# Kernel tuning notes

Hardware: AMD Instinct MI355X
Metric: run time of the kernel (lower is better)

The kernel has to match this reference:

```python
import jax, jax.numpy as jnp
import numpy as np

HEADS = 8
RANK = 4

def _lora(x, w_down, w_up, palette, in_dim, out_dim):
    # w_down: [RANK*in_dim, 15], w_up: [RANK*out_dim, 15], palette: [1, 15]
    down = (palette @ w_down.T).reshape(RANK, in_dim)   # [r, in]
    up = (palette @ w_up.T).reshape(out_dim, RANK)      # [out, r]
    return (x @ down.T) @ up.T                          # [..., out]


def setup_inputs() -> dict:
    key = jax.random.key(0)
    ks = jax.random.split(key, 16)
    B, S, D = 2, 2048, 1280
    def n(k, shape, std=0.02):
        return (jax.random.normal(k, shape, dtype=jnp.float32) * std).astype(jnp.float32)
    return {
        'hidden_states': jax.random.normal(ks[0], (B, S, D), dtype=jnp.float32),
        'color_palette': jax.random.uniform(ks[1], (1, 15), dtype=jnp.float32),
        'Wq': n(ks[2], (D, D)), 'Wk': n(ks[3], (D, D)),
        'Wv': n(ks[4], (D, D)), 'Wo': n(ks[5], (D, D)),
        'bo': jnp.zeros((D,), dtype=jnp.float32),
        'q_down': n(ks[6], (RANK * D, 15), 0.25), 'q_up': n(ks[7], (RANK * D, 15)),
        'k_down': n(ks[8], (RANK * D, 15), 0.25), 'k_up': n(ks[9], (RANK * D, 15)),
        'v_down': n(ks[10], (RANK * D, 15), 0.25), 'v_up': n(ks[11], (RANK * D, 15)),
        'o_down': n(ks[12], (RANK * D, 15), 0.25), 'o_up': n(ks[13], (RANK * D, 15)),
    }


def reference(hidden_states, color_palette, Wq, Wk, Wv, Wo, bo,
              q_down, q_up, k_down, k_up, v_down, v_up, o_down, o_up):
    B, S, D = hidden_states.shape
    H = HEADS
    hd = D // H
    scale = 1.0  # LoRA scale
    x = hidden_states
    # LoRA-augmented projections (self-attention: encoder_hidden_states = x)
    q = x @ Wq.T + scale * _lora(x, q_down, q_up, color_palette, D, D)
    k = x @ Wk.T + scale * _lora(x, k_down, k_up, color_palette, D, D)
    v = x @ Wv.T + scale * _lora(x, v_down, v_up, color_palette, D, D)
    # split heads: [B, S, D] -> [B, H, S, hd]
    q = q.reshape(B, S, H, hd).transpose(0, 2, 1, 3)
    k = k.reshape(B, S, H, hd).transpose(0, 2, 1, 3)
    v = v.reshape(B, S, H, hd).transpose(0, 2, 1, 3)
    attn_scale = 1.0 / jnp.sqrt(jnp.asarray(hd, dtype=q.dtype))
    scores = jnp.einsum('bhqd,bhkd->bhqk', q, k) * attn_scale
    probs = jax.nn.softmax(scores, axis=-1)
    out = jnp.einsum('bhqk,bhkd->bhqd', probs, v)
    out = out.transpose(0, 2, 1, 3).reshape(B, S, D)
    out = out @ Wo.T + bo + scale * _lora(out, o_down, o_up, color_palette, D, D)
    return out
```

## Files before the change

kernel.cpp:

```cpp
#include <hip/hip_runtime.h>

typedef unsigned short u16;
typedef unsigned int u32;
typedef __attribute__((ext_vector_type(4))) float floatx4;
typedef __attribute__((ext_vector_type(8))) __bf16 bf16x8;

#define MFMA_BF16(a, b, c) __builtin_amdgcn_mfma_f32_16x16x32_bf16((a), (b), (c), 0, 0, 0)

typedef const __attribute__((address_space(1))) void* gas_ptr;
typedef __attribute__((address_space(3))) void* las_ptr;

__device__ __forceinline__ void gll16(const void* g, void* l) {
  __builtin_amdgcn_global_load_lds((gas_ptr)g, (las_ptr)l, 16, 0, 0);
}

__device__ __forceinline__ u16 f2bf(float x) {
  u32 u = __builtin_bit_cast(u32, x);
  u = (u + 0x7fffu + ((u >> 16) & 1u)) >> 16;
  return (u16)u;
}

__global__ void prep_downup(const float* __restrict__ pal,
                            const float* __restrict__ qd, const float* __restrict__ qu,
                            const float* __restrict__ kd, const float* __restrict__ ku,
                            const float* __restrict__ vd, const float* __restrict__ vu,
                            const float* __restrict__ od, const float* __restrict__ ou,
                            float* __restrict__ down_f, float* __restrict__ up_f) {
  int tid = blockIdx.x * blockDim.x + threadIdx.x;
  int w = tid / 10240;
  int rem = tid - w * 10240;
  const float* dsrc = (w == 0) ? qd : (w == 1) ? kd : (w == 2) ? vd : od;
  const float* usrc = (w == 0) ? qu : (w == 1) ? ku : (w == 2) ? vu : ou;
  bool isdown = rem < 5120;
  int row = isdown ? rem : rem - 5120;
  const float* src = (isdown ? dsrc : usrc) + row * 15;
  float s = 0.f;
#pragma unroll
  for (int p = 0; p < 15; ++p) s += pal[p] * src[p];
  if (isdown) down_f[w * 5120 + row] = s;
  else        up_f[w * 5120 + row] = s;
}

__global__ void build_weff(const float* __restrict__ Wq, const float* __restrict__ Wk,
                           const float* __restrict__ Wv, const float* __restrict__ Wo,
                           const float* __restrict__ down_f, const float* __restrict__ up_f,
                           u16* __restrict__ weff_qkv, u16* __restrict__ weff_o) {
  int tid = blockIdx.x * blockDim.x + threadIdx.x;
  int w = tid / 1638400;
  int rem = tid - w * 1638400;
  int n = rem / 1280;
  int k = rem - n * 1280;
  const float* W = (w == 0) ? Wq : (w == 1) ? Wk : (w == 2) ? Wv : Wo;
  const float* up = up_f + w * 5120 + n * 4;
  const float* dn = down_f + w * 5120 + k;
  float v = W[rem] + up[0] * dn[0] + up[1] * dn[1280] + up[2] * dn[2560] + up[3] * dn[3840];
  u16 hv = f2bf(v);
  if (w < 3) weff_qkv[w * 1638400 + rem] = hv;
  else       weff_o[rem] = hv;
}

__global__ void cvt_x(const float4* __restrict__ x, ushort4* __restrict__ xb) {
  int i = blockIdx.x * blockDim.x + threadIdx.x;
  float4 v = x[i];
  ushort4 o;
  o.x = f2bf(v.x); o.y = f2bf(v.y); o.z = f2bf(v.z); o.w = f2bf(v.w);
  xb[i] = o;
}

__global__ __launch_bounds__(256) void gemm128_qkv(const u16* __restrict__ A, const u16* __restrict__ Bm,
                                                   u16* __restrict__ qb, u16* __restrict__ kb,
                                                   u16* __restrict__ vbuf, int K) {
  __shared__ __align__(16) u16 lA[128 * 64];
  __shared__ __align__(16) u16 lB[128 * 64];
  const int t = threadIdx.x;
  const int lane = t & 63;
  const int l15 = lane & 15, quad = lane >> 4;
  const int wid = t >> 6;
  const int wm = (wid >> 1) * 64;
  const int wn = (wid & 1) * 64;
  const int bm = blockIdx.x * 128;
  const int bn = blockIdx.y * 128;
  floatx4 acc[4][4] = {};

  int soff[4];
#pragma unroll
  for (int i = 0; i < 4; ++i) {
    int c = t + i * 256;
    int row = c >> 3, pos = c & 7;
    soff[i] = row * K + ((pos + row) & 7) * 8;
  }
  int afo[4][2], bfo[4][2];
#pragma unroll
  for (int i = 0; i < 4; ++i) {
#pragma unroll
    for (int ch = 0; ch < 2; ++ch) {
      int ra = wm + i * 16 + l15;
      int rb = wn + i * 16 + l15;
      int kc8 = ch * 4 + quad;
      afo[i][ch] = ra * 64 + ((kc8 - ra) & 7) * 8;
      bfo[i][ch] = rb * 64 + ((kc8 - rb) & 7) * 8;
    }
  }

  const u16* Ab = A + (long)bm * K;
  const u16* Bb = Bm + (long)bn * K;
  const int nkt = K >> 6;

  for (int kt = 0; kt < nkt; ++kt) {
    __syncthreads();
    const int k0 = kt * 64;
#pragma unroll
    for (int i = 0; i < 4; ++i) gll16(Ab + (long)soff[i] + k0, lA + (t + i * 256) * 8);
#pragma unroll
    for (int i = 0; i < 4; ++i) gll16(Bb + (long)soff[i] + k0, lB + (t + i * 256) * 8);
    __syncthreads();
#pragma unroll
    for (int ch = 0; ch < 2; ++ch) {
      bf16x8 af[4], bfr[4];
#pragma unroll
      for (int i = 0; i < 4; ++i) af[i] = *(const bf16x8*)(lA + afo[i][ch]);
#pragma unroll
      for (int i = 0; i < 4; ++i) bfr[i] = *(const bf16x8*)(lB + bfo[i][ch]);
#pragma unroll
      for (int i = 0; i < 4; ++i)
#pragma unroll
        for (int j = 0; j < 4; ++j)
          acc[i][j] = MFMA_BF16(af[i], bfr[j], acc[i][j]);
    }
  }

#pragma unroll
  for (int i = 0; i < 4; ++i) {
#pragma unroll
    for (int j = 0; j < 4; ++j) {
#pragma unroll
      for (int r = 0; r < 4; ++r) {
        int m = bm + wm + i * 16 + quad * 4 + r;
        int n = bn + wn + j * 16 + l15;
        u16 hv = f2bf(acc[i][j][r]);
        if (n < 1280) {
          qb[(long)m * 1280 + n] = hv;
        } else if (n < 2560) {
          kb[(long)m * 1280 + (n - 1280)] = hv;
        } else {
          vbuf[(long)m * 1280 + (n - 2560)] = hv;
        }
      }
    }
  }
}

__global__ __launch_bounds__(256) void vtrans(const u16* __restrict__ vbuf,
                                              u16* __restrict__ vtb) {
  __shared__ u16 tile[64 * 65];
  const int t = threadIdx.x;
  const int sb = blockIdx.x * 64, nb = blockIdx.y * 64, b = blockIdx.z;
  const u16* src = vbuf + ((long)(b * 2048 + sb)) * 1280 + nb;
#pragma unroll
  for (int it = 0; it < 16; ++it) {
    int idx = t + it * 256;
    int s = idx >> 6, n = idx & 63;
    tile[s * 65 + n] = src[(long)s * 1280 + n];
  }
  __syncthreads();
  u16* dst = vtb + ((long)(b * 1280 + nb)) * 2048 + sb;
#pragma unroll
  for (int it = 0; it < 16; ++it) {
    int idx = t + it * 256;
    int n = idx >> 6, s = idx & 63;
    dst[(long)n * 2048 + s] = tile[s * 65 + n];
  }
}

__global__ __launch_bounds__(256) void gemm64_o(const u16* __restrict__ A, const u16* __restrict__ Bm,
                                                float* __restrict__ outf,
                                                const float* __restrict__ bias, int K) {
  __shared__ __align__(16) u16 lA[64 * 64];
  __shared__ __align__(16) u16 lB[128 * 64];
  const int t = threadIdx.x;
  const int lane = t & 63;
  const int l15 = lane & 15, quad = lane >> 4;
  const int wid = t >> 6;
  const int bm = blockIdx.x * 64;
  const int bn = blockIdx.y * 128;
  floatx4 acc[4][2] = {};

  int aoff[2], boff[4];
#pragma unroll
  for (int i = 0; i < 2; ++i) {
    int c = t + i * 256;
    int row = c >> 3, pos = c & 7;
    aoff[i] = row * K + ((pos + row) & 7) * 8;
  }
#pragma unroll
  for (int i = 0; i < 4; ++i) {
    int c = t + i * 256;
    int row = c >> 3, pos = c & 7;
    boff[i] = row * K + ((pos + row) & 7) * 8;
  }
  int afo[4][2], bfo[2][2];
#pragma unroll
  for (int ch = 0; ch < 2; ++ch) {
    int kc8 = ch * 4 + quad;
#pragma unroll
    for (int i = 0; i < 4; ++i) {
      int ra = i * 16 + l15;
      afo[i][ch] = ra * 64 + ((kc8 - ra) & 7) * 8;
    }
#pragma unroll
    for (int j = 0; j < 2; ++j) {
      int rb = wid * 32 + j * 16 + l15;
      bfo[j][ch] = rb * 64 + ((kc8 - rb) & 7) * 8;
    }
  }

  const u16* Ab = A + (long)bm * K;
  const u16* Bb = Bm + (long)bn * K;
  const int nkt = K >> 6;

  for (int kt = 0; kt < nkt; ++kt) {
    __syncthreads();
    const int k0 = kt * 64;
#pragma unroll
    for (int i = 0; i < 2; ++i) gll16(Ab + (long)aoff[i] + k0, lA + (t + i * 256) * 8);
#pragma unroll
    for (int i = 0; i < 4; ++i) gll16(Bb + (long)boff[i] + k0, lB + (t + i * 256) * 8);
    __syncthreads();
#pragma unroll
    for (int ch = 0; ch < 2; ++ch) {
      bf16x8 af[4], bfr[2];
#pragma unroll
      for (int i = 0; i < 4; ++i) af[i] = *(const bf16x8*)(lA + afo[i][ch]);
#pragma unroll
      for (int j = 0; j < 2; ++j) bfr[j] = *(const bf16x8*)(lB + bfo[j][ch]);
#pragma unroll
      for (int i = 0; i < 4; ++i)
#pragma unroll
        for (int j = 0; j < 2; ++j)
          acc[i][j] = MFMA_BF16(af[i], bfr[j], acc[i][j]);
    }
  }

#pragma unroll
  for (int i = 0; i < 4; ++i) {
#pragma unroll
    for (int j = 0; j < 2; ++j) {
#pragma unroll
      for (int r = 0; r < 4; ++r) {
        int m = bm + i * 16 + quad * 4 + r;
        int n = bn + wid * 32 + j * 16 + l15;
        outf[(long)m * 1280 + n] = acc[i][j][r] + bias[n];
      }
    }
  }
}

__global__ __launch_bounds__(256) void flash_attn(const u16* __restrict__ qb,
                                                  const u16* __restrict__ kb,
                                                  const u16* __restrict__ vtb,
                                                  u16* __restrict__ attn) {
  const int S = 2048, D = 1280, HD = 160;
  __shared__ __align__(16) u16 kt_lds[64 * 160];
  __shared__ __align__(16) u16 vt_lds[160 * 64];
  __shared__ __align__(16) u16 p_lds[4][16 * 76];
  const int t = threadIdx.x, lane = t & 63, wid = t >> 6;
  const int quad = lane >> 4, l15 = lane & 15;
  const int bh = blockIdx.y, b = bh >> 3, h = bh & 7;
  const int q0 = blockIdx.x * 64 + wid * 16;
  const float kS = 0.11404582025f;

  bf16x8 aq[5];
  {
    const u16* qg = qb + ((long)(b * 2048 + q0 + l15)) * D + h * HD + quad * 8;
#pragma unroll
    for (int dc = 0; dc < 5; ++dc) aq[dc] = *(const bf16x8*)(qg + dc * 32);
  }

  const u16* kg[5];
  const u16* vg[5];
  {
    const u16* kgbase = kb + ((long)(b * 2048)) * D + h * HD;
    const u16* vgbase = vtb + ((long)(b * 1280 + h * HD)) * 2048;
#pragma unroll
    for (int i = 0; i < 5; ++i) {
      int c = t + i * 256;
      int key = c / 20, rot = c - key * 20;
      int ccol = rot - (key % 20);
      if (ccol < 0) ccol += 20;
      kg[i] = kgbase + (long)key * D + ccol * 8;
      int vrow = c >> 3, swz = c & 7;
      int vcol = swz ^ (vrow & 7);
      vg[i] = vgbase + (long)vrow * 2048 + vcol * 8;
    }
  }

  int kfo[4][5];
#pragma unroll
  for (int j = 0; j < 4; ++j) {
    int key = j * 16 + l15;
    int r0 = (quad + key) % 20;
#pragma unroll
    for (int dc = 0; dc < 5; ++dc) {
      int rot = r0 + dc * 4;
      if (rot >= 20) rot -= 20;
      kfo[j][dc] = (key * 20 + rot) * 8;
    }
  }
  int vfo[10][2];
#pragma unroll
  for (int dc = 0; dc < 10; ++dc) {
    int row = dc * 16 + l15;
#pragma unroll
    for (int ks = 0; ks < 2; ++ks) {
      int sw = (ks * 4 + quad) ^ (row & 7);
      vfo[dc][ks] = (row * 8 + sw) * 8;
    }
  }

  float l_part[4] = {0.f, 0.f, 0.f, 0.f};
  floatx4 o_acc[10] = {};

  for (int kt0 = 0; kt0 < S; kt0 += 64) {
    __syncthreads();
#pragma unroll
    for (int i = 0; i < 5; ++i) gll16(kg[i], kt_lds + (t + i * 256) * 8);
#pragma unroll
    for (int i = 0; i < 5; ++i) gll16(vg[i], vt_lds + (t + i * 256) * 8);
#pragma unroll
    for (int i = 0; i < 5; ++i) { kg[i] += (long)64 * D; vg[i] += 64; }
    __syncthreads();

    floatx4 s[4] = {};
#pragma unroll
    for (int dc = 0; dc < 5; ++dc) {
#pragma unroll
      for (int j = 0; j < 4; ++j) {
        bf16x8 kf = *(const bf16x8*)(kt_lds + kfo[j][dc]);
        s[j] = MFMA_BF16(aq[dc], kf, s[j]);
      }
    }

#pragma unroll
    for (int r = 0; r < 4; ++r) {
      float p0 = __builtin_exp2f(fminf(s[0][r] * kS, 80.f));
      float p1 = __builtin_exp2f(fminf(s[1][r] * kS, 80.f));
      float p2 = __builtin_exp2f(fminf(s[2][r] * kS, 80.f));
      float p3 = __builtin_exp2f(fminf(s[3][r] * kS, 80.f));
      l_part[r] += (p0 + p1) + (p2 + p3);
      u16* pw = p_lds[wid] + (quad * 4 + r) * 76 + l15;
      pw[0]  = f2bf(p0);
      pw[16] = f2bf(p1);
      pw[32] = f2bf(p2);
      pw[48] = f2bf(p3);
    }
    asm volatile("s_waitcnt lgkmcnt(0)" ::: "memory");

    bf16x8 paA = *(const bf16x8*)(p_lds[wid] + l15 * 76 + quad * 8);
    bf16x8 paB = *(const bf16x8*)(p_lds[wid] + l15 * 76 + 32 + quad * 8);
#pragma unroll
    for (int dc = 0; dc < 10; ++dc) {
      bf16x8 vfA = *(const bf16x8*)(vt_lds + vfo[dc][0]);
      bf16x8 vfB = *(const bf16x8*)(vt_lds + vfo[dc][1]);
      o_acc[dc] = MFMA_BF16(paA, vfA, o_acc[dc]);
      o_acc[dc] = MFMA_BF16(paB, vfB, o_acc[dc]);
    }
  }

  float rl[4];
#pragma unroll
  for (int r = 0; r < 4; ++r) {
    float rs = l_part[r];
    rs += __shfl_xor(rs, 1, 64);
    rs += __shfl_xor(rs, 2, 64);
    rs += __shfl_xor(rs, 4, 64);
    rs += __shfl_xor(rs, 8, 64);
    rl[r] = 1.0f / rs;
  }
#pragma unroll
  for (int dc = 0; dc < 10; ++dc) {
#pragma unroll
    for (int r = 0; r < 4; ++r) {
      float v = o_acc[dc][r] * rl[r];
      int row = q0 + quad * 4 + r;
      int col = h * HD + dc * 16 + l15;
      attn[((long)(b * 2048 + row)) * D + col] = f2bf(v);
    }
  }
}

extern "C" void kernel_launch(void* const* d_in, const int* in_sizes, int n_in,
                              void* d_out, int out_size, void* d_ws, size_t ws_size,
                              hipStream_t stream) {
  const float* x   = (const float*)d_in[0];
  const float* pal = (const float*)d_in[1];
  const float* Wq  = (const float*)d_in[2];
  const float* Wk  = (const float*)d_in[3];
  const float* Wv  = (const float*)d_in[4];
  const float* Wo  = (const float*)d_in[5];
  const float* bo  = (const float*)d_in[6];
  const float* qd  = (const float*)d_in[7];
  const float* qu  = (const float*)d_in[8];
  const float* kd  = (const float*)d_in[9];
  const float* ku  = (const float*)d_in[10];
  const float* vd  = (const float*)d_in[11];
  const float* vu  = (const float*)d_in[12];
  const float* od  = (const float*)d_in[13];
  const float* ou  = (const float*)d_in[14];
  float* out = (float*)d_out;

  char* ws = (char*)d_ws;
  u16* xb       = (u16*)(ws);
  u16* weff_qkv = (u16*)(ws + 10485760);
  u16* weff_o   = (u16*)(ws + 20316160);
  u16* qbuf     = (u16*)(ws + 23592960);
  u16* kbuf     = (u16*)(ws + 34078720);
  u16* vtb      = (u16*)(ws + 44564480);
  u16* attn     = (u16*)(ws + 55050240);
  float* down_f = (float*)(ws + 65536000);
  float* up_f   = (float*)(ws + 65617920);
  u16* vbuf     = (u16*)(ws + 65699840);

  prep_downup<<<160, 256, 0, stream>>>(pal, qd, qu, kd, ku, vd, vu, od, ou, down_f, up_f);
  build_weff<<<25600, 256, 0, stream>>>(Wq, Wk, Wv, Wo, down_f, up_f, weff_qkv, weff_o);
  cvt_x<<<5120, 256, 0, stream>>>((const float4*)x, (ushort4*)xb);
  gemm128_qkv<<<dim3(32, 30), 256, 0, stream>>>(xb, weff_qkv, qbuf, kbuf, vbuf, 1280);
  vtrans<<<dim3(32, 20, 2), 256, 0, stream>>>(vbuf, vtb);
  flash_attn<<<dim3(32, 16), 256, 0, stream>>>(qbuf, kbuf, vtb, attn);
  gemm64_o<<<dim3(64, 10), 256, 0, stream>>>(attn, weff_o, out, bo, 1280);
}
```

Baseline: 298.7 us.

## Double-buffer K/V tiles in flash attention with 512-thread blocks

The flash attention kernel now uses 8 waves per block, each handling 16 queries, so 128 queries per block share every K/V tile load. K and V tiles are double-buffered in LDS, with the next tile's async global-to-LDS loads issued before computing on the current one, and the wait uses vmcnt instead of a full barrier pair. This is meant to hide global load latency and halve K/V traffic per query, at the cost of doubled LDS (about 90KB) and only 256 blocks, which may reduce occupancy and grid fill on the device.

```diff
diff --git a/kernel.cpp b/kernel.cpp
--- a/kernel.cpp
+++ b/kernel.cpp
@@ -255,18 +255,17 @@
   }
 }
 
-__global__ __launch_bounds__(256) void flash_attn(const u16* __restrict__ qb,
+__global__ __launch_bounds__(512) void flash_attn(const u16* __restrict__ qb,
                                                   const u16* __restrict__ kb,
                                                   const u16* __restrict__ vtb,
                                                   u16* __restrict__ attn) {
   const int S = 2048, D = 1280, HD = 160;
-  __shared__ __align__(16) u16 kt_lds[64 * 160];
-  __shared__ __align__(16) u16 vt_lds[160 * 64];
-  __shared__ __align__(16) u16 p_lds[4][16 * 76];
+  __shared__ __align__(16) u16 kv_lds[2][64 * 160 + 160 * 64];
+  __shared__ __align__(16) u16 p_lds[8][16 * 76];
   const int t = threadIdx.x, lane = t & 63, wid = t >> 6;
   const int quad = lane >> 4, l15 = lane & 15;
   const int bh = blockIdx.y, b = bh >> 3, h = bh & 7;
-  const int q0 = blockIdx.x * 64 + wid * 16;
+  const int q0 = blockIdx.x * 128 + wid * 16;
   const float kS = 0.11404582025f;
 
   bf16x8 aq[5];
@@ -276,21 +275,23 @@
     for (int dc = 0; dc < 5; ++dc) aq[dc] = *(const bf16x8*)(qg + dc * 32);
   }
 
-  const u16* kg[5];
-  const u16* vg[5];
-  {
-    const u16* kgbase = kb + ((long)(b * 2048)) * D + h * HD;
-    const u16* vgbase = vtb + ((long)(b * 1280 + h * HD)) * 2048;
-#pragma unroll
-    for (int i = 0; i < 5; ++i) {
-      int c = t + i * 256;
-      int key = c / 20, rot = c - key * 20;
-      int ccol = rot - (key % 20);
+  const u16* sg[5];
+  int sadv[5];
+#pragma unroll
+  for (int i = 0; i < 5; ++i) {
+    int c = t + i * 512;
+    if (c < 1280) {
+      int key = c / 20, pos = c - key * 20;
+      int ccol = pos - (key % 20);
       if (ccol < 0) ccol += 20;
-      kg[i] = kgbase + (long)key * D + ccol * 8;
-      int vrow = c >> 3, swz = c & 7;
+      sg[i] = kb + ((long)(b * 2048 + key)) * D + h * HD + ccol * 8;
+      sadv[i] = 64 * D;
+    } else {
+      int c2 = c - 1280;
+      int vrow = c2 >> 3, swz = c2 & 7;
       int vcol = swz ^ (vrow & 7);
-      vg[i] = vgbase + (long)vrow * 2048 + vcol * 8;
+      sg[i] = vtb + ((long)(b * 1280 + h * HD + vrow)) * 2048 + vcol * 8;
+      sadv[i] = 64;
     }
   }
 
@@ -313,29 +314,41 @@
 #pragma unroll
     for (int ks = 0; ks < 2; ++ks) {
       int sw = (ks * 4 + quad) ^ (row & 7);
-      vfo[dc][ks] = (row * 8 + sw) * 8;
+      vfo[dc][ks] = 10240 + (row * 8 + sw) * 8;
     }
   }
 
   float l_part[4] = {0.f, 0.f, 0.f, 0.f};
   floatx4 o_acc[10] = {};
 
-  for (int kt0 = 0; kt0 < S; kt0 += 64) {
-    __syncthreads();
-#pragma unroll
-    for (int i = 0; i < 5; ++i) gll16(kg[i], kt_lds + (t + i * 256) * 8);
-#pragma unroll
-    for (int i = 0; i < 5; ++i) gll16(vg[i], vt_lds + (t + i * 256) * 8);
-#pragma unroll
-    for (int i = 0; i < 5; ++i) { kg[i] += (long)64 * D; vg[i] += 64; }
-    __syncthreads();
+#pragma unroll
+  for (int i = 0; i < 5; ++i) {
+    gll16(sg[i], &kv_lds[0][0] + (t + i * 512) * 8);
+    sg[i] += sadv[i];
+  }
+
+  for (int kt0 = 0; kt0 < 32; ++kt0) {
+    u16* cbase = &kv_lds[kt0 & 1][0];
+    if (kt0 < 31) {
+      u16* nbase = &kv_lds[(kt0 & 1) ^ 1][0];
+#pragma unroll
+      for (int i = 0; i < 5; ++i) {
+        gll16(sg[i], nbase + (t + i * 512) * 8);
+        sg[i] += sadv[i];
+      }
+      asm volatile("s_waitcnt vmcnt(5)" ::: "memory");
+    } else {
+      asm volatile("s_waitcnt vmcnt(0)" ::: "memory");
+    }
+    __builtin_amdgcn_s_barrier();
+    __builtin_amdgcn_sched_barrier(0);
 
     floatx4 s[4] = {};
 #pragma unroll
     for (int dc = 0; dc < 5; ++dc) {
 #pragma unroll
       for (int j = 0; j < 4; ++j) {
-        bf16x8 kf = *(const bf16x8*)(kt_lds + kfo[j][dc]);
+        bf16x8 kf = *(const bf16x8*)(cbase + kfo[j][dc]);
         s[j] = MFMA_BF16(aq[dc], kf, s[j]);
       }
     }
@@ -359,11 +372,13 @@
     bf16x8 paB = *(const bf16x8*)(p_lds[wid] + l15 * 76 + 32 + quad * 8);
 #pragma unroll
     for (int dc = 0; dc < 10; ++dc) {
-      bf16x8 vfA = *(const bf16x8*)(vt_lds + vfo[dc][0]);
-      bf16x8 vfB = *(const bf16x8*)(vt_lds + vfo[dc][1]);
+      bf16x8 vfA = *(const bf16x8*)(cbase + vfo[dc][0]);
+      bf16x8 vfB = *(const bf16x8*)(cbase + vfo[dc][1]);
       o_acc[dc] = MFMA_BF16(paA, vfA, o_acc[dc]);
       o_acc[dc] = MFMA_BF16(paB, vfB, o_acc[dc]);
     }
+    __builtin_amdgcn_sched_barrier(0);
+    __builtin_amdgcn_s_barrier();
   }
 
   float rl[4];
@@ -425,6 +440,6 @@
   cvt_x<<<5120, 256, 0, stream>>>((const float4*)x, (ushort4*)xb);
   gemm128_qkv<<<dim3(32, 30), 256, 0, stream>>>(xb, weff_qkv, qbuf, kbuf, vbuf, 1280);
   vtrans<<<dim3(32, 20, 2), 256, 0, stream>>>(vbuf, vtb);
-  flash_attn<<<dim3(32, 16), 256, 0, stream>>>(qbuf, kbuf, vtb, attn);
+  flash_attn<<<dim3(16, 16), 512, 0, stream>>>(qbuf, kbuf, vtb, attn);
   gemm64_o<<<dim3(64, 10), 256, 0, stream>>>(attn, weff_o, out, bo, 1280);
 }
```

Result: no change. 303.7 us (+1.7%).
